# Performance work log

Hardware: AMD Instinct MI355X
Metric: run time of the kernel (lower is better)

Reference implementation:

```python
import math
import jax, jax.numpy as jnp
import numpy as np

# Module config (from init_kwargs): hidden_size=128, num_heads=8, dropout=0.0
HIDDEN = 128
HEADS = 8
HEAD_DIM = HIDDEN // HEADS  # 16
SCALE = math.sqrt(HEAD_DIM)  # sqrt(hidden_size_per_attention_head)
B = 1
N = 50000   # nodes
E = 800000  # edges


def setup_inputs() -> dict:
    key = jax.random.key(0)
    k1, k2, k3, k4 = jax.random.split(key, 4)
    q = jax.random.normal(k1, (B, N, HIDDEN), dtype=jnp.float32)
    k = jax.random.normal(k2, (B, N, HIDDEN), dtype=jnp.float32)
    v = jax.random.normal(k3, (B, N, HIDDEN), dtype=jnp.float32)
    edge_index = jax.random.randint(k4, (2, E), 0, N, dtype=jnp.int64)
    return {"q": q, "k": k, "v": v, "edge_index": edge_index}


def reference(q, k, v, edge_index):
    # sparse_attention_bias path (attn_type='sparse', attn_bias=None)
    batch, node_num, _ = q.shape
    total = batch * node_num
    qh = q.reshape(total, HEADS, HEAD_DIM)
    kh = k.reshape(total, HEADS, HEAD_DIM)
    vh = v.reshape(total, HEADS, HEAD_DIM)

    e_src = edge_index[0]   # gathers k, v
    e_dst = edge_index[1]   # gathers q, scatter target

    # per-edge, per-head score: [E, H, 1]
    score = jnp.sum(kh[e_src] * qh[e_dst], axis=-1, keepdims=True) / SCALE
    score = jnp.exp(jnp.clip(score, -5.0, 5.0))

    msg = vh[e_src] * score                                   # [E, H, D]
    wV = jax.ops.segment_sum(msg, e_dst, num_segments=total)   # [N, H, D]
    Z = jax.ops.segment_sum(score, e_dst, num_segments=total)  # [N, H, 1]

    x = wV / (Z + 1e-6)
    return x.reshape(batch, node_num, -1)
```

## Files before the change

kernel.cpp:

```cpp
#include <hip/hip_runtime.h>

#define HEADS 8
#define HEAD_DIM 16
#define HIDDEN 128
#define CAP 64

__device__ __forceinline__ unsigned pack2_bf16(float a, float b) {
    unsigned ua = __float_as_uint(a);
    unsigned ub = __float_as_uint(b);
    ua = (ua + 0x7fffu + ((ua >> 16) & 1u)) >> 16;
    ub = (ub + 0x7fffu + ((ub >> 16) & 1u)) >> 16;
    return ua | (ub << 16);
}
__device__ __forceinline__ float bflo(unsigned u) { return __uint_as_float(u << 16); }
__device__ __forceinline__ float bfhi(unsigned u) { return __uint_as_float(u & 0xffff0000u); }

__global__ void prep_kernel(const int* __restrict__ ei, int E,
                            const float* __restrict__ k, const float* __restrict__ v,
                            int* __restrict__ cursor, int* __restrict__ perm,
                            unsigned* __restrict__ kb, unsigned* __restrict__ vb,
                            int fill_blocks, int nvec ) {
    if ((int)blockIdx.x < fill_blocks) {
        __shared__ int is64_s;
        if (threadIdx.x < 64) {
            int nz = ei[2 * (int)threadIdx.x + 1];
            nz |= __shfl_xor(nz, 1);
            nz |= __shfl_xor(nz, 2);
            nz |= __shfl_xor(nz, 4);
            nz |= __shfl_xor(nz, 8);
            nz |= __shfl_xor(nz, 16);
            nz |= __shfl_xor(nz, 32);
            if (threadIdx.x == 0) is64_s = (nz == 0);
        }
        __syncthreads();
        int e = blockIdx.x * blockDim.x + threadIdx.x;
        if (e >= E) return;
        int src, dst;
        if (is64_s) {
            const long long* e64 = (const long long*)ei;
            src = (int)e64[e];
            dst = (int)e64[(long long)E + e];
        } else {
            src = ei[e];
            dst = ei[E + e];
        }
        int pos = atomicAdd(&cursor[dst], 1);
        if (pos < CAP) perm[(dst << 6) + pos] = src;
    } else {
        int t = (blockIdx.x - fill_blocks) * blockDim.x + threadIdx.x;
        if (t >= 2 * nvec) return;
        int arr = (t >= nvec) ? 1 : 0;
        int i = arr ? t - nvec : t;
        const float4* s4 = (const float4*)(arr ? v : k);
        float4 a = s4[2 * i];
        float4 b = s4[2 * i + 1];
        uint4 o;
        o.x = pack2_bf16(a.x, a.y);
        o.y = pack2_bf16(a.z, a.w);
        o.z = pack2_bf16(b.x, b.y);
        o.w = pack2_bf16(b.z, b.w);
        ((uint4*)(arr ? vb : kb))[i] = o;
    }
}

__global__ __launch_bounds__(256) void gather_bf16_kernel(
        const float* __restrict__ q,
        const uint4* __restrict__ kb4, const uint4* __restrict__ vb4,
        const int* __restrict__ cursor, const int* __restrict__ perm,
        float* __restrict__ out, int N) {
    int node = blockIdx.x * 8 + ((int)threadIdx.x >> 5);
    int l = threadIdx.x & 31;
    int half = l >> 4;
    int sl = l & 15;
    if (node >= N) return;

    const float4* qp = (const float4*)q;
    float4 qa = qp[node * 32 + sl * 2];
    float4 qb = qp[node * 32 + sl * 2 + 1];
    float q0 = qa.x * 0.25f, q1 = qa.y * 0.25f, q2 = qa.z * 0.25f, q3 = qa.w * 0.25f;
    float q4 = qb.x * 0.25f, q5 = qb.y * 0.25f, q6 = qb.z * 0.25f, q7 = qb.w * 0.25f;

    int deg = cursor[node];
    if (deg > CAP) deg = CAP;
    int beg = node << 6;
    int end = beg + deg;

    float a0 = 0.f, a1 = 0.f, a2 = 0.f, a3 = 0.f, a4 = 0.f, a5 = 0.f, a6 = 0.f, a7 = 0.f;
    float zacc = 0.f;

    for (int i = beg; i < end; i += 2) {
        int idx = i + half;
        if (idx < end) {
            int s = perm[idx];
            uint4 kw = kb4[s * 16 + sl];
            float p = bflo(kw.x) * q0 + bfhi(kw.x) * q1 + bflo(kw.y) * q2 + bfhi(kw.y) * q3
                    + bflo(kw.z) * q4 + bfhi(kw.z) * q5 + bflo(kw.w) * q6 + bfhi(kw.w) * q7;
            p += __shfl_xor(p, 1);
            float e = __expf(fminf(fmaxf(p, -5.f), 5.f));
            uint4 vw = vb4[s * 16 + sl];
            a0 += bflo(vw.x) * e;
            a1 += bfhi(vw.x) * e;
            a2 += bflo(vw.y) * e;
            a3 += bfhi(vw.y) * e;
            a4 += bflo(vw.z) * e;
            a5 += bfhi(vw.z) * e;
            a6 += bflo(vw.w) * e;
            a7 += bfhi(vw.w) * e;
            zacc += e;
        }
    }
    a0 += __shfl_xor(a0, 16);
    a1 += __shfl_xor(a1, 16);
    a2 += __shfl_xor(a2, 16);
    a3 += __shfl_xor(a3, 16);
    a4 += __shfl_xor(a4, 16);
    a5 += __shfl_xor(a5, 16);
    a6 += __shfl_xor(a6, 16);
    a7 += __shfl_xor(a7, 16);
    zacc += __shfl_xor(zacc, 16);

    if (half == 0) {
        float inv = 1.0f / (zacc + 1e-6f);
        float4* out4 = (float4*)out;
        out4[node * 32 + sl * 2]     = make_float4(a0 * inv, a1 * inv, a2 * inv, a3 * inv);
        out4[node * 32 + sl * 2 + 1] = make_float4(a4 * inv, a5 * inv, a6 * inv, a7 * inv);
    }
}

__global__ void fill_fixed_kernel(const int* __restrict__ ei, int* __restrict__ cursor,
                                  int* __restrict__ perm, int E) {
    __shared__ int is64_s;
    if (threadIdx.x < 64) {
        int nz = ei[2 * (int)threadIdx.x + 1];
        nz |= __shfl_xor(nz, 1);
        nz |= __shfl_xor(nz, 2);
        nz |= __shfl_xor(nz, 4);
        nz |= __shfl_xor(nz, 8);
        nz |= __shfl_xor(nz, 16);
        nz |= __shfl_xor(nz, 32);
        if (threadIdx.x == 0) is64_s = (nz == 0);
    }
    __syncthreads();
    int e = blockIdx.x * blockDim.x + threadIdx.x;
    if (e >= E) return;
    int src, dst;
    if (is64_s) {
        const long long* e64 = (const long long*)ei;
        src = (int)e64[e];
        dst = (int)e64[(long long)E + e];
    } else {
        src = ei[e];
        dst = ei[E + e];
    }
    int pos = atomicAdd(&cursor[dst], 1);
    if (pos < CAP) perm[(dst << 6) + pos] = src;
}

__global__ void gather_fixed_kernel(const float* __restrict__ q, const float* __restrict__ k,
                                    const float* __restrict__ v,
                                    const int* __restrict__ cursor, const int* __restrict__ perm,
                                    float* __restrict__ out, int N) {
    int node = blockIdx.x * (blockDim.x >> 5) + ((int)threadIdx.x >> 5);
    int l = threadIdx.x & 31;
    if (node >= N) return;
    const float4* q4 = (const float4*)q;
    const float4* k4 = (const float4*)k;
    const float4* v4 = (const float4*)v;
    float4 qv = q4[node * 32 + l];
    int deg = cursor[node];
    if (deg > CAP) deg = CAP;
    int beg = node << 6;
    int end = beg + deg;
    float4 acc = make_float4(0.f, 0.f, 0.f, 0.f);
    float zacc = 0.f;
    int i = beg;
    for (; i + 2 <= end; i += 2) {
        int s0 = perm[i];
        int s1 = perm[i + 1];
        float4 ka = k4[s0 * 32 + l];
        float4 va = v4[s0 * 32 + l];
        float4 kb = k4[s1 * 32 + l];
        float4 vb = v4[s1 * 32 + l];
        float pa = ka.x * qv.x + ka.y * qv.y + ka.z * qv.z + ka.w * qv.w;
        float pb = kb.x * qv.x + kb.y * qv.y + kb.z * qv.z + kb.w * qv.w;
        pa += __shfl_xor(pa, 1);
        pa += __shfl_xor(pa, 2);
        pb += __shfl_xor(pb, 1);
        pb += __shfl_xor(pb, 2);
        float ea = __expf(fminf(fmaxf(pa * 0.25f, -5.f), 5.f));
        float eb = __expf(fminf(fmaxf(pb * 0.25f, -5.f), 5.f));
        acc.x += va.x * ea + vb.x * eb;
        acc.y += va.y * ea + vb.y * eb;
        acc.z += va.z * ea + vb.z * eb;
        acc.w += va.w * ea + vb.w * eb;
        zacc += ea + eb;
    }
    if (i < end) {
        int s0 = perm[i];
        float4 ka = k4[s0 * 32 + l];
        float4 va = v4[s0 * 32 + l];
        float pa = ka.x * qv.x + ka.y * qv.y + ka.z * qv.z + ka.w * qv.w;
        pa += __shfl_xor(pa, 1);
        pa += __shfl_xor(pa, 2);
        float ea = __expf(fminf(fmaxf(pa * 0.25f, -5.f), 5.f));
        acc.x += va.x * ea;
        acc.y += va.y * ea;
        acc.z += va.z * ea;
        acc.w += va.w * ea;
        zacc += ea;
    }
    float zr = zacc + 1e-6f;
    ((float4*)out)[node * 32 + l] =
        make_float4(acc.x / zr, acc.y / zr, acc.z / zr, acc.w / zr);
}

extern "C" void kernel_launch(void* const* d_in, const int* in_sizes, int n_in,
                              void* d_out, int out_size, void* d_ws, size_t ws_size,
                              hipStream_t stream) {
    const float* q = (const float*)d_in[0];
    const float* k = (const float*)d_in[1];
    const float* v = (const float*)d_in[2];
    const int* ei  = (const int*)d_in[3];

    int N = in_sizes[0] / HIDDEN;
    int E = in_sizes[3] / 2;
    float* out = (float*)d_out;

    int block = 256;
    int nvec = N * HIDDEN / 8;

    size_t need_bf16 = (size_t)N * sizeof(int) + (size_t)N * CAP * sizeof(int)
                     + 2 * (size_t)nvec * sizeof(uint4);
    size_t need_f32  = (size_t)N * sizeof(int) + (size_t)N * CAP * sizeof(int);

    int* cursor = (int*)d_ws;
    int* perm   = cursor + N;

    if (ws_size >= need_bf16) {
        unsigned* kb = (unsigned*)(perm + (size_t)N * CAP);
        unsigned* vb = kb + (size_t)nvec * 4;
        hipMemsetAsync(cursor, 0, (size_t)N * sizeof(int), stream);
        int FB = (E + block - 1) / block;
        int CB = (2 * nvec + block - 1) / block;
        prep_kernel<<<FB + CB, block, 0, stream>>>(ei, E, k, v, cursor, perm, kb, vb, FB, nvec);
        gather_bf16_kernel<<<(N + 7) / 8, 256, 0, stream>>>(
            q, (const uint4*)kb, (const uint4*)vb, cursor, perm, out, N);
    } else if (ws_size >= need_f32) {
        hipMemsetAsync(cursor, 0, (size_t)N * sizeof(int), stream);
        fill_fixed_kernel<<<(E + block - 1) / block, block, 0, stream>>>(ei, cursor, perm, E);
        gather_fixed_kernel<<<(N + 7) / 8, 256, 0, stream>>>(q, k, v, cursor, perm, out, N);
    }
}
```

Baseline: 236.8 us.

## Interleave bf16 K and V rows and process four edges per wavefront

The prep kernel now writes K and V in bf16 into one interleaved buffer, so each source node's 256-byte K row sits next to its V row. The 0.25 scale is folded into K during packing instead of being applied to q in the gather. The gather kernel gives each node a full 64-lane wavefront that handles four edges per iteration instead of two, with an extra shuffle stage in the reduction. This aims to improve locality of the per-edge K/V fetches and raise memory-level parallelism, at the cost of fewer nodes per block and more idle lanes for low-degree nodes.

```diff
diff --git a/kernel.cpp b/kernel.cpp
--- a/kernel.cpp
+++ b/kernel.cpp
@@ -18,8 +18,8 @@
 __global__ void prep_kernel(const int* __restrict__ ei, int E,
                             const float* __restrict__ k, const float* __restrict__ v,
                             int* __restrict__ cursor, int* __restrict__ perm,
-                            unsigned* __restrict__ kb, unsigned* __restrict__ vb,
-                            int fill_blocks, int nvec ) {
+                            uint4* __restrict__ kv,
+                            int fill_blocks, int total_vecs ) {
     if ((int)blockIdx.x < fill_blocks) {
         __shared__ int is64_s;
         if (threadIdx.x < 64) {
@@ -48,37 +48,39 @@
         if (pos < CAP) perm[(dst << 6) + pos] = src;
     } else {
         int t = (blockIdx.x - fill_blocks) * blockDim.x + threadIdx.x;
-        if (t >= 2 * nvec) return;
-        int arr = (t >= nvec) ? 1 : 0;
-        int i = arr ? t - nvec : t;
-        const float4* s4 = (const float4*)(arr ? v : k);
-        float4 a = s4[2 * i];
-        float4 b = s4[2 * i + 1];
+        if (t >= total_vecs) return;
+        int row  = t >> 5;
+        int slot = t & 31;
+        int j    = slot & 15;
+        const float4* s4 = (const float4*)((slot < 16) ? k : v);
+        float4 a = s4[(long long)row * 32 + j * 2];
+        float4 b = s4[(long long)row * 32 + j * 2 + 1];
+        if (slot < 16) {
+            a.x *= 0.25f; a.y *= 0.25f; a.z *= 0.25f; a.w *= 0.25f;
+            b.x *= 0.25f; b.y *= 0.25f; b.z *= 0.25f; b.w *= 0.25f;
+        }
         uint4 o;
         o.x = pack2_bf16(a.x, a.y);
         o.y = pack2_bf16(a.z, a.w);
         o.z = pack2_bf16(b.x, b.y);
         o.w = pack2_bf16(b.z, b.w);
-        ((uint4*)(arr ? vb : kb))[i] = o;
-    }
-}
-
-__global__ __launch_bounds__(256) void gather_bf16_kernel(
-        const float* __restrict__ q,
-        const uint4* __restrict__ kb4, const uint4* __restrict__ vb4,
+        kv[t] = o;
+    }
+}
+
+__global__ __launch_bounds__(256) void gather_kv_kernel(
+        const float* __restrict__ q, const uint4* __restrict__ kv,
         const int* __restrict__ cursor, const int* __restrict__ perm,
         float* __restrict__ out, int N) {
-    int node = blockIdx.x * 8 + ((int)threadIdx.x >> 5);
-    int l = threadIdx.x & 31;
-    int half = l >> 4;
+    int node = blockIdx.x * 4 + ((int)threadIdx.x >> 6);
+    int l = threadIdx.x & 63;
+    int quarter = l >> 4;
     int sl = l & 15;
     if (node >= N) return;
 
     const float4* qp = (const float4*)q;
     float4 qa = qp[node * 32 + sl * 2];
     float4 qb = qp[node * 32 + sl * 2 + 1];
-    float q0 = qa.x * 0.25f, q1 = qa.y * 0.25f, q2 = qa.z * 0.25f, q3 = qa.w * 0.25f;
-    float q4 = qb.x * 0.25f, q5 = qb.y * 0.25f, q6 = qb.z * 0.25f, q7 = qb.w * 0.25f;
 
     int deg = cursor[node];
     if (deg > CAP) deg = CAP;
@@ -88,16 +90,19 @@
     float a0 = 0.f, a1 = 0.f, a2 = 0.f, a3 = 0.f, a4 = 0.f, a5 = 0.f, a6 = 0.f, a7 = 0.f;
     float zacc = 0.f;
 
-    for (int i = beg; i < end; i += 2) {
-        int idx = i + half;
+    for (int i = beg; i < end; i += 4) {
+        int idx = i + quarter;
         if (idx < end) {
             int s = perm[idx];
-            uint4 kw = kb4[s * 16 + sl];
-            float p = bflo(kw.x) * q0 + bfhi(kw.x) * q1 + bflo(kw.y) * q2 + bfhi(kw.y) * q3
-                    + bflo(kw.z) * q4 + bfhi(kw.z) * q5 + bflo(kw.w) * q6 + bfhi(kw.w) * q7;
+            const uint4* base = kv + (size_t)s * 32 + sl;
+            uint4 kw = base[0];
+            uint4 vw = base[16];
+            float p = bflo(kw.x) * qa.x + bfhi(kw.x) * qa.y
+                    + bflo(kw.y) * qa.z + bfhi(kw.y) * qa.w
+                    + bflo(kw.z) * qb.x + bfhi(kw.z) * qb.y
+                    + bflo(kw.w) * qb.z + bfhi(kw.w) * qb.w;
             p += __shfl_xor(p, 1);
             float e = __expf(fminf(fmaxf(p, -5.f), 5.f));
-            uint4 vw = vb4[s * 16 + sl];
             a0 += bflo(vw.x) * e;
             a1 += bfhi(vw.x) * e;
             a2 += bflo(vw.y) * e;
@@ -109,17 +114,17 @@
             zacc += e;
         }
     }
-    a0 += __shfl_xor(a0, 16);
-    a1 += __shfl_xor(a1, 16);
-    a2 += __shfl_xor(a2, 16);
-    a3 += __shfl_xor(a3, 16);
-    a4 += __shfl_xor(a4, 16);
-    a5 += __shfl_xor(a5, 16);
-    a6 += __shfl_xor(a6, 16);
-    a7 += __shfl_xor(a7, 16);
-    zacc += __shfl_xor(zacc, 16);
-
-    if (half == 0) {
+    a0 += __shfl_xor(a0, 16); a0 += __shfl_xor(a0, 32);
+    a1 += __shfl_xor(a1, 16); a1 += __shfl_xor(a1, 32);
+    a2 += __shfl_xor(a2, 16); a2 += __shfl_xor(a2, 32);
+    a3 += __shfl_xor(a3, 16); a3 += __shfl_xor(a3, 32);
+    a4 += __shfl_xor(a4, 16); a4 += __shfl_xor(a4, 32);
+    a5 += __shfl_xor(a5, 16); a5 += __shfl_xor(a5, 32);
+    a6 += __shfl_xor(a6, 16); a6 += __shfl_xor(a6, 32);
+    a7 += __shfl_xor(a7, 16); a7 += __shfl_xor(a7, 32);
+    zacc += __shfl_xor(zacc, 16); zacc += __shfl_xor(zacc, 32);
+
+    if (quarter == 0) {
         float inv = 1.0f / (zacc + 1e-6f);
         float4* out4 = (float4*)out;
         out4[node * 32 + sl * 2]     = make_float4(a0 * inv, a1 * inv, a2 * inv, a3 * inv);
@@ -227,24 +232,22 @@
     float* out = (float*)d_out;
 
     int block = 256;
-    int nvec = N * HIDDEN / 8;
-
-    size_t need_bf16 = (size_t)N * sizeof(int) + (size_t)N * CAP * sizeof(int)
-                     + 2 * (size_t)nvec * sizeof(uint4);
-    size_t need_f32  = (size_t)N * sizeof(int) + (size_t)N * CAP * sizeof(int);
+    int total_vecs = N * 32;
+
+    size_t need_kv  = (size_t)N * sizeof(int) + (size_t)N * CAP * sizeof(int)
+                    + (size_t)total_vecs * sizeof(uint4);
+    size_t need_f32 = (size_t)N * sizeof(int) + (size_t)N * CAP * sizeof(int);
 
     int* cursor = (int*)d_ws;
     int* perm   = cursor + N;
 
-    if (ws_size >= need_bf16) {
-        unsigned* kb = (unsigned*)(perm + (size_t)N * CAP);
-        unsigned* vb = kb + (size_t)nvec * 4;
+    if (ws_size >= need_kv) {
+        uint4* kv = (uint4*)(perm + (size_t)N * CAP);
         hipMemsetAsync(cursor, 0, (size_t)N * sizeof(int), stream);
         int FB = (E + block - 1) / block;
-        int CB = (2 * nvec + block - 1) / block;
-        prep_kernel<<<FB + CB, block, 0, stream>>>(ei, E, k, v, cursor, perm, kb, vb, FB, nvec);
-        gather_bf16_kernel<<<(N + 7) / 8, 256, 0, stream>>>(
-            q, (const uint4*)kb, (const uint4*)vb, cursor, perm, out, N);
+        int CB = (total_vecs + block - 1) / block;
+        prep_kernel<<<FB + CB, block, 0, stream>>>(ei, E, k, v, cursor, perm, kv, FB, total_vecs);
+        gather_kv_kernel<<<(N + 3) / 4, 256, 0, stream>>>(q, kv, cursor, perm, out, N);
     } else if (ws_size >= need_f32) {
         hipMemsetAsync(cursor, 0, (size_t)N * sizeof(int), stream);
         fill_fixed_kernel<<<(E + block - 1) / block, block, 0, stream>>>(ei, cursor, perm, E);
```

Measured after the change: 223.1 us. 5.8% less time.
